# Optimization experiments

Measured on AMD Instinct MI355X. Metric: run time of the kernel, lower is better.

## Reference

```python
import jax, jax.numpy as jnp
import numpy as np

D_MODEL = 768
NUM_HEADS = 12
D_K = D_MODEL // NUM_HEADS  # 64


def setup_inputs() -> dict:
    key = jax.random.key(0)
    ks = jax.random.split(key, 7)
    B, S = 2, 4096
    Q = jax.random.normal(ks[0], (B, S, D_MODEL), dtype=jnp.float32)
    K = jax.random.normal(ks[1], (B, S, D_MODEL), dtype=jnp.float32)
    V = jax.random.normal(ks[2], (B, S, D_MODEL), dtype=jnp.float32)
    scale = 1.0 / np.sqrt(D_MODEL)
    # Per-head projection weights stacked: [H, d_model, d_k] (equivalent to
    # the torch per-head nn.Linear(d_model, d_k, bias=False) applied as x @ W)
    WQ = jax.random.normal(ks[3], (NUM_HEADS, D_MODEL, D_K), dtype=jnp.float32) * scale
    WK = jax.random.normal(ks[4], (NUM_HEADS, D_MODEL, D_K), dtype=jnp.float32) * scale
    WV = jax.random.normal(ks[5], (NUM_HEADS, D_MODEL, D_K), dtype=jnp.float32) * scale
    # Output projection: [num_head*d_v, d_model]
    WO = jax.random.normal(ks[6], (NUM_HEADS * D_K, D_MODEL), dtype=jnp.float32) * scale
    return {"Q": Q, "K": K, "V": V, "WQ": WQ, "WK": WK, "WV": WV, "WO": WO}


def reference(Q, K, V, WQ, WK, WV, WO):
    # Per-head projections (batched over heads): [B,H,S,d_k]
    q = jnp.einsum('bsd,hdk->bhsk', Q, WQ)
    k = jnp.einsum('bsd,hdk->bhsk', K, WK)
    v = jnp.einsum('bsd,hdk->bhsk', V, WV)
    # Full attention scores: [B,H,S,S]
    scores = jnp.einsum('bhqd,bhsd->bhqs', q, k) / jnp.sqrt(jnp.asarray(D_K, q.dtype))
    attn = jax.nn.softmax(scores, axis=-1)  # dropout_p=0 -> identity
    out = jnp.einsum('bhqs,bhsd->bhqd', attn, v)  # [B,H,S,d_k]
    # Concatenate heads along feature dim (head order = concat order)
    B, H, S, Dk = out.shape
    out = out.transpose(0, 2, 1, 3).reshape(B, S, H * Dk)
    return out @ WO  # [B,S,d_model]
```

## Files before the change

kernel.cpp:

```cpp
#include <hip/hip_runtime.h>
#include <hip/hip_bf16.h>
#include <stdint.h>
#include <stddef.h>

#define NH 12
#define DKH 64
#define DM 768
#define SS 4096

typedef __attribute__((ext_vector_type(8))) short bf16x8;
typedef __attribute__((ext_vector_type(4))) float f32x4;
typedef __attribute__((ext_vector_type(16))) float f32x16;

__device__ __forceinline__ unsigned short f2bf(float x) {
  union { float f; unsigned int u; } a; a.f = x;
  unsigned int r = a.u + 0x7fffu + ((a.u >> 16) & 1u);
  return (unsigned short)(r >> 16);
}

__device__ __forceinline__ unsigned pkbf2(float a, float b) {
  union { __hip_bfloat162 h; unsigned u; } x;
  x.h = __float22bfloat162_rn(float2{a, b});
  return x.u;
}

__device__ __forceinline__ unsigned cvt_pk_bf16(float lo, float hi) {
  unsigned r;
  asm("v_cvt_pk_bf16_f32 %0, %1, %2" : "=v"(r) : "v"(lo), "v"(hi));
  return r;
}

__device__ __forceinline__ void plane32_swap(unsigned& a, unsigned& b) {
  asm("v_permlane32_swap_b32 %0, %1" : "+v"(a), "+v"(b));
}

__device__ __forceinline__ float fast_exp2(float x) {
#if __has_builtin(__builtin_amdgcn_exp2f)
  return __builtin_amdgcn_exp2f(x);
#else
  return exp2f(x);
#endif
}

__device__ __forceinline__ void gload16(const void* g, void* l) {
  __builtin_amdgcn_global_load_lds(
      (const __attribute__((address_space(1))) void*)g,
      (__attribute__((address_space(3))) void*)l, 16, 0, 0);
}

__global__ __launch_bounds__(256) void conv_weights(
    const float* __restrict__ WQ, const float* __restrict__ WK,
    const float* __restrict__ WV, const float* __restrict__ WO,
    unsigned short* __restrict__ wq, unsigned short* __restrict__ wk,
    unsigned short* __restrict__ wv, unsigned short* __restrict__ wo) {
  int idx = blockIdx.x * 256 + threadIdx.x;
  if (idx >= DM * DM) return;
  int n = idx / DM, k = idx % DM;
  int src = ((n >> 6) * DM + k) * DKH + (n & 63);
  wq[idx] = f2bf(WQ[src] * 0.18033688011112042f);
  wk[idx] = f2bf(WK[src]);
  wv[idx] = f2bf(WV[src]);
  wo[idx] = f2bf(WO[k * DM + n]);
}

__global__ __launch_bounds__(256) void qkv_conv(
    const float* __restrict__ Q, const float* __restrict__ K,
    const float* __restrict__ V, unsigned short* __restrict__ out) {
  int gid = blockIdx.x * 256 + threadIdx.x;
  int t = gid / 786432, e = gid % 786432;
  const float* src = (t == 0) ? Q : (t == 1) ? K : V;
  float4 a = *(const float4*)(src + (size_t)e * 8);
  float4 c = *(const float4*)(src + (size_t)e * 8 + 4);
  union { unsigned u[4]; uint4 v; } o;
  o.u[0] = pkbf2(a.x, a.y); o.u[1] = pkbf2(a.z, a.w);
  o.u[2] = pkbf2(c.x, c.y); o.u[3] = pkbf2(c.z, c.w);
  *(uint4*)(out + (size_t)t * 6291456 + (size_t)e * 8) = o.v;
}

__global__ __launch_bounds__(256, 2) void proj_gemm3(
    const unsigned short* __restrict__ Abase,
    const unsigned short* __restrict__ Wbase,
    unsigned short* __restrict__ Obase) {
  __shared__ unsigned short As[2][128 * 64];
  __shared__ unsigned short Bs[2][96 * 64];
  const int tid = threadIdx.x;
  const int lane = tid & 63, wave = tid >> 6;
  const int wm = wave >> 1, wn = wave & 1;
  const int l15 = lane & 15, lhi = lane >> 4;
  const int lrow = lane >> 3;
  const int schunk = (lane & 7) ^ lrow;

  int fid = blockIdx.x + (blockIdx.y << 3) + (blockIdx.z << 9);
  int nid = (fid & 7) * 192 + (fid >> 3);
  const int bx = nid & 7;
  const int rem = nid >> 3;
  const int by = rem & 63, z = rem >> 6;
  const bool z2 = (z == 2);

  const unsigned short* A = Abase + (size_t)z * 6291456;
  const unsigned short* Wt = Wbase + (size_t)z * DM * DM;
  unsigned short* out = Obase + (size_t)z * 2 * NH * SS * DKH;
  const int m0 = by * 128, n0 = bx * 96;

  auto stage = [&](int k0, int buf) {
#pragma unroll
    for (int i = 0; i < 4; ++i) {
      int r = wave * 32 + i * 8;
      gload16(A + (size_t)(m0 + r + lrow) * DM + k0 + schunk * 8, &As[buf][r * 64]);
    }
#pragma unroll
    for (int i = 0; i < 3; ++i) {
      int r = wave * 24 + i * 8;
      gload16(Wt + (size_t)(n0 + r + lrow) * DM + k0 + schunk * 8, &Bs[buf][r * 64]);
    }
  };

  f32x4 acc[4][3] = {};

  stage(0, 0);
  stage(64, 1);

  for (int t = 0; t < 12; ++t) {
    if (t < 11) asm volatile("s_waitcnt vmcnt(7)" ::: "memory");
    else        asm volatile("s_waitcnt vmcnt(0)" ::: "memory");
    asm volatile("s_barrier" ::: "memory");
    const int buf = t & 1;
    bf16x8 af[4][2], bfr[3][2];
#pragma unroll
    for (int m = 0; m < 4; ++m) {
      int row = wm * 64 + m * 16 + l15;
#pragma unroll
      for (int ks = 0; ks < 2; ++ks)
        af[m][ks] = *(const bf16x8*)&As[buf][row * 64 + (((ks * 4 + lhi) ^ (row & 7)) * 8)];
    }
#pragma unroll
    for (int n = 0; n < 3; ++n) {
      int row = wn * 48 + n * 16 + l15;
#pragma unroll
      for (int ks = 0; ks < 2; ++ks)
        bfr[n][ks] = *(const bf16x8*)&Bs[buf][row * 64 + (((ks * 4 + lhi) ^ (row & 7)) * 8)];
    }
    asm volatile("s_waitcnt lgkmcnt(0)" ::: "memory");
    asm volatile("s_barrier" ::: "memory");
    if (t + 2 < 12) stage((t + 2) * 64, buf);
    __builtin_amdgcn_s_setprio(1);
#pragma unroll
    for (int ks = 0; ks < 2; ++ks)
#pragma unroll
      for (int m = 0; m < 4; ++m)
#pragma unroll
        for (int n = 0; n < 3; ++n) {
          if (z2)
            acc[m][n] = __builtin_amdgcn_mfma_f32_16x16x32_bf16(bfr[n][ks], af[m][ks], acc[m][n], 0, 0, 0);
          else
            acc[m][n] = __builtin_amdgcn_mfma_f32_16x16x32_bf16(af[m][ks], bfr[n][ks], acc[m][n], 0, 0, 0);
        }
    __builtin_amdgcn_s_setprio(0);
  }

  if (!z2) {
#pragma unroll
    for (int m = 0; m < 4; ++m) {
#pragma unroll
      for (int r = 0; r < 4; ++r) {
        int row = m0 + wm * 64 + m * 16 + lhi * 4 + r;
        int bb = row >> 12, s = row & 4095;
#pragma unroll
        for (int n = 0; n < 3; ++n) {
          int col = n0 + wn * 48 + n * 16 + l15;
          int hh = col >> 6, dk = col & 63;
          out[((size_t)(bb * NH + hh) * SS + s) * DKH + dk] = f2bf(acc[m][n][r]);
        }
      }
    }
  } else {
#pragma unroll
    for (int m = 0; m < 4; ++m) {
      int srow = m0 + wm * 64 + m * 16 + l15;
      int bb = srow >> 12, s = srow & 4095;
#pragma unroll
      for (int n = 0; n < 3; ++n) {
#pragma unroll
        for (int r = 0; r < 4; ++r) {
          int col = n0 + wn * 48 + n * 16 + lhi * 4 + r;
          int hh = col >> 6, dk = col & 63;
          out[((size_t)(bb * NH + hh) * DKH + dk) * SS + s] = f2bf(acc[m][n][r]);
        }
      }
    }
  }
}

__device__ __forceinline__ void pack_pb(const f32x16& s0, const f32x16& s1, bf16x8* pb) {
#pragma unroll
  for (int h2 = 0; h2 < 2; ++h2) {
    unsigned c0a = cvt_pk_bf16(s0[8 * h2 + 0], s0[8 * h2 + 1]);
    unsigned c1a = cvt_pk_bf16(s0[8 * h2 + 2], s0[8 * h2 + 3]);
    unsigned c0b = cvt_pk_bf16(s0[8 * h2 + 4], s0[8 * h2 + 5]);
    unsigned c1b = cvt_pk_bf16(s0[8 * h2 + 6], s0[8 * h2 + 7]);
    plane32_swap(c0a, c0b);
    plane32_swap(c1a, c1b);
    union { unsigned u[4]; bf16x8 v; } f;
    f.u[0] = c0a; f.u[1] = c1a; f.u[2] = c0b; f.u[3] = c1b;
    pb[h2] = f.v;
  }
#pragma unroll
  for (int h2 = 0; h2 < 2; ++h2) {
    unsigned c0a = cvt_pk_bf16(s1[8 * h2 + 0], s1[8 * h2 + 1]);
    unsigned c1a = cvt_pk_bf16(s1[8 * h2 + 2], s1[8 * h2 + 3]);
    unsigned c0b = cvt_pk_bf16(s1[8 * h2 + 4], s1[8 * h2 + 5]);
    unsigned c1b = cvt_pk_bf16(s1[8 * h2 + 6], s1[8 * h2 + 7]);
    plane32_swap(c0a, c0b);
    plane32_swap(c1a, c1b);
    union { unsigned u[4]; bf16x8 v; } f;
    f.u[0] = c0a; f.u[1] = c1a; f.u[2] = c0b; f.u[3] = c1b;
    pb[2 + h2] = f.v;
  }
}

__device__ __forceinline__ float tree16(const f32x16& v) {
  float a = (v[0] + v[1]) + (v[2] + v[3]);
  float b = (v[4] + v[5]) + (v[6] + v[7]);
  float c = (v[8] + v[9]) + (v[10] + v[11]);
  float d = (v[12] + v[13]) + (v[14] + v[15]);
  return (a + b) + (c + d);
}

__global__ __launch_bounds__(256, 2) void flash_attn(
    const unsigned short* __restrict__ Qp, const unsigned short* __restrict__ Kp,
    const unsigned short* __restrict__ Vt, unsigned short* __restrict__ Ao) {
  __shared__ unsigned short LDSu[2][2][8192];
  float* Ob = (float*)&LDSu[0][0][0];
  float* Lb = (float*)&LDSu[1][0][0];
  const int tid = threadIdx.x;
  const int lane = tid & 63, wave = tid >> 6;
  const int pair = wave >> 1, wp = wave & 1;
  const int ql = lane & 31, hi = lane >> 5;

  int fid = blockIdx.x + (blockIdx.y << 5);
  int nid = (fid & 7) * 96 + (fid >> 3);
  const int bx = nid & 31, bh = nid >> 5;
  const int b = bh / NH, h = bh % NH;
  const int q0 = bx * 128 + wp * 64;
  const int kvbase = pair * (SS / 2);

  bf16x8 qf0[4], qf1[4];
  {
    const unsigned short* qb = Qp + ((size_t)bh * SS + q0 + ql) * DKH;
#pragma unroll
    for (int s = 0; s < 4; ++s) {
      qf0[s] = *(const bf16x8*)(qb + s * 16 + hi * 8);
      qf1[s] = *(const bf16x8*)(qb + 32 * DKH + s * 16 + hi * 8);
    }
  }

  const unsigned short* gK = Kp + (size_t)bh * SS * DKH;
  const unsigned short* gV = Vt + (size_t)bh * DKH * SS;
  const int lrow = lane >> 3;
  const int sch = ((lane & 7) ^ lrow) * 8;
  const int xs = (ql & 7) << 3;

  unsigned short* KV0 = &LDSu[pair][0][0];
  unsigned short* KV1 = &LDSu[pair][1][0];

#pragma unroll
  for (int i = 0; i < 4; ++i) {
    int r = wp * 32 + i * 8;
    gload16(gK + (size_t)(kvbase + r + lrow) * DKH + sch, KV0 + r * 64);
    gload16(gV + (size_t)(r + lrow) * SS + kvbase + sch, KV0 + 4096 + r * 64);
  }

  f32x16 oA = {}, oB = {}, oC = {}, oD = {};
  float lp0 = 0.f, lp1 = 0.f;

  for (int it = 0; it < 32; ++it) {
    asm volatile("s_waitcnt vmcnt(0)" ::: "memory");
    __builtin_amdgcn_s_barrier();
    __builtin_amdgcn_sched_barrier(0);
    unsigned short* cur = (it & 1) ? KV1 : KV0;
    unsigned short* nxt = (it & 1) ? KV0 : KV1;
    if (it + 1 < 32) {
      int kvn = kvbase + (it + 1) * 64;
#pragma unroll
      for (int i = 0; i < 4; ++i) {
        int r = wp * 32 + i * 8;
        gload16(gK + (size_t)(kvn + r + lrow) * DKH + sch, nxt + r * 64);
        gload16(gV + (size_t)(r + lrow) * SS + kvn + sch, nxt + 4096 + r * 64);
      }
    }
    const unsigned short* Ks = cur;
    const unsigned short* Vs = cur + 4096;

    f32x16 s00 = {}, s01 = {}, s10 = {}, s11 = {};
    __builtin_amdgcn_s_setprio(1);
#pragma unroll
    for (int s = 0; s < 4; ++s) {
      bf16x8 ka0 = *(const bf16x8*)&Ks[ql * 64 + ((s * 16 + hi * 8) ^ xs)];
      bf16x8 ka1 = *(const bf16x8*)&Ks[(32 + ql) * 64 + ((s * 16 + hi * 8) ^ xs)];
      s00 = __builtin_amdgcn_mfma_f32_32x32x16_bf16(ka0, qf0[s], s00, 0, 0, 0);
      s10 = __builtin_amdgcn_mfma_f32_32x32x16_bf16(ka0, qf1[s], s10, 0, 0, 0);
      s01 = __builtin_amdgcn_mfma_f32_32x32x16_bf16(ka1, qf0[s], s01, 0, 0, 0);
      s11 = __builtin_amdgcn_mfma_f32_32x32x16_bf16(ka1, qf1[s], s11, 0, 0, 0);
    }
    __builtin_amdgcn_s_setprio(0);

#pragma unroll
    for (int r = 0; r < 16; ++r) s00[r] = fast_exp2(s00[r]);
#pragma unroll
    for (int r = 0; r < 16; ++r) s01[r] = fast_exp2(s01[r]);
#pragma unroll
    for (int r = 0; r < 16; ++r) s10[r] = fast_exp2(s10[r]);
#pragma unroll
    for (int r = 0; r < 16; ++r) s11[r] = fast_exp2(s11[r]);
    lp0 += tree16(s00) + tree16(s01);
    lp1 += tree16(s10) + tree16(s11);

    bf16x8 pb0[4], pb1[4];
    pack_pb(s00, s01, pb0);
    pack_pb(s10, s11, pb1);

    __builtin_amdgcn_s_setprio(1);
#pragma unroll
    for (int ks = 0; ks < 4; ++ks) {
      bf16x8 va0 = *(const bf16x8*)&Vs[ql * 64 + ((ks * 16 + hi * 8) ^ xs)];
      bf16x8 va1 = *(const bf16x8*)&Vs[(32 + ql) * 64 + ((ks * 16 + hi * 8) ^ xs)];
      oA = __builtin_amdgcn_mfma_f32_32x32x16_bf16(va0, pb0[ks], oA, 0, 0, 0);
      oB = __builtin_amdgcn_mfma_f32_32x32x16_bf16(va1, pb0[ks], oB, 0, 0, 0);
      oC = __builtin_amdgcn_mfma_f32_32x32x16_bf16(va0, pb1[ks], oC, 0, 0, 0);
      oD = __builtin_amdgcn_mfma_f32_32x32x16_bf16(va1, pb1[ks], oD, 0, 0, 0);
    }
    __builtin_amdgcn_s_setprio(0);
  }

  float l0 = lp0 + __shfl_xor(lp0, 32);
  float l1 = lp1 + __shfl_xor(lp1, 32);
  const int qq0 = wp * 64 + ql, qq1 = wp * 64 + 32 + ql;
  const int swz0 = (qq0 & 7) << 3, swz1 = (qq1 & 7) << 3;

  __syncthreads();
  if (pair == 0) {
#pragma unroll
    for (int g = 0; g < 4; ++g) {
      int d0 = hi * 4 + g * 8;
      *(float4*)&Ob[qq0 * 64 + (d0 ^ swz0)] = float4{oA[4 * g], oA[4 * g + 1], oA[4 * g + 2], oA[4 * g + 3]};
      *(float4*)&Ob[qq0 * 64 + ((d0 + 32) ^ swz0)] = float4{oB[4 * g], oB[4 * g + 1], oB[4 * g + 2], oB[4 * g + 3]};
      *(float4*)&Ob[qq1 * 64 + (d0 ^ swz1)] = float4{oC[4 * g], oC[4 * g + 1], oC[4 * g + 2], oC[4 * g + 3]};
      *(float4*)&Ob[qq1 * 64 + ((d0 + 32) ^ swz1)] = float4{oD[4 * g], oD[4 * g + 1], oD[4 * g + 2], oD[4 * g + 3]};
    }
    if (hi == 0) { Lb[qq0] = l0; Lb[qq1] = l1; }
  }
  __syncthreads();
  if (pair == 1) {
    float inv0 = 1.0f / (l0 + Lb[qq0]);
    float inv1 = 1.0f / (l1 + Lb[qq1]);
#pragma unroll
    for (int g = 0; g < 4; ++g) {
      int d0 = hi * 4 + g * 8;
      float4 pA = *(const float4*)&Ob[qq0 * 64 + (d0 ^ swz0)];
      float4 pB = *(const float4*)&Ob[qq0 * 64 + ((d0 + 32) ^ swz0)];
      float4 pC = *(const float4*)&Ob[qq1 * 64 + (d0 ^ swz1)];
      float4 pD = *(const float4*)&Ob[qq1 * 64 + ((d0 + 32) ^ swz1)];
      oA[4 * g] += pA.x; oA[4 * g + 1] += pA.y; oA[4 * g + 2] += pA.z; oA[4 * g + 3] += pA.w;
      oB[4 * g] += pB.x; oB[4 * g + 1] += pB.y; oB[4 * g + 2] += pB.z; oB[4 * g + 3] += pB.w;
      oC[4 * g] += pC.x; oC[4 * g + 1] += pC.y; oC[4 * g + 2] += pC.z; oC[4 * g + 3] += pC.w;
      oD[4 * g] += pD.x; oD[4 * g + 1] += pD.y; oD[4 * g + 2] += pD.z; oD[4 * g + 3] += pD.w;
    }
    unsigned short* orow0 = Ao + ((size_t)b * SS + q0 + ql) * DM + h * DKH;
    unsigned short* orow1 = Ao + ((size_t)b * SS + q0 + 32 + ql) * DM + h * DKH;
#pragma unroll
    for (int g = 0; g < 4; ++g) {
      int d0 = g * 8 + hi * 4;
      *(unsigned*)&orow0[d0]          = cvt_pk_bf16(oA[4 * g + 0] * inv0, oA[4 * g + 1] * inv0);
      *(unsigned*)&orow0[d0 + 2]      = cvt_pk_bf16(oA[4 * g + 2] * inv0, oA[4 * g + 3] * inv0);
      *(unsigned*)&orow0[32 + d0]     = cvt_pk_bf16(oB[4 * g + 0] * inv0, oB[4 * g + 1] * inv0);
      *(unsigned*)&orow0[32 + d0 + 2] = cvt_pk_bf16(oB[4 * g + 2] * inv0, oB[4 * g + 3] * inv0);
      *(unsigned*)&orow1[d0]          = cvt_pk_bf16(oC[4 * g + 0] * inv1, oC[4 * g + 1] * inv1);
      *(unsigned*)&orow1[d0 + 2]      = cvt_pk_bf16(oC[4 * g + 2] * inv1, oC[4 * g + 3] * inv1);
      *(unsigned*)&orow1[32 + d0]     = cvt_pk_bf16(oD[4 * g + 0] * inv1, oD[4 * g + 1] * inv1);
      *(unsigned*)&orow1[32 + d0 + 2] = cvt_pk_bf16(oD[4 * g + 2] * inv1, oD[4 * g + 3] * inv1);
    }
  }
}

__global__ __launch_bounds__(256, 2) void out_gemm(
    const unsigned short* __restrict__ A, const unsigned short* __restrict__ Wt,
    float* __restrict__ out) {
  __shared__ unsigned short As[2][64 * 64];
  __shared__ unsigned short Bs[2][128 * 64];
  const int tid = threadIdx.x;
  const int lane = tid & 63, wave = tid >> 6;
  const int wm = wave >> 1, wn = wave & 1;
  const int l15 = lane & 15, lhi = lane >> 4;
  const int lrow = lane >> 3;
  const int schunk = (lane & 7) ^ lrow;

  int fid = blockIdx.x + 6 * blockIdx.y;
  int nid = (fid & 7) * 96 + (fid >> 3);
  const int bx = nid % 6, by = nid / 6;
  const int m0 = by * 64, n0 = bx * 128;

  auto stage = [&](int k0, int buf) {
#pragma unroll
    for (int i = 0; i < 4; ++i) {
      int r = wave * 32 + i * 8;
      gload16(Wt + (size_t)(n0 + r + lrow) * DM + k0 + schunk * 8, &Bs[buf][r * 64]);
    }
#pragma unroll
    for (int i = 0; i < 2; ++i) {
      int r = wave * 16 + i * 8;
      gload16(A + (size_t)(m0 + r + lrow) * DM + k0 + schunk * 8, &As[buf][r * 64]);
    }
  };

  f32x4 acc[2][4] = {};
  stage(0, 0);
  stage(64, 1);

  for (int t = 0; t < 12; ++t) {
    if (t < 11) asm volatile("s_waitcnt vmcnt(6)" ::: "memory");
    else        asm volatile("s_waitcnt vmcnt(0)" ::: "memory");
    asm volatile("s_barrier" ::: "memory");
    const int buf = t & 1;
    bf16x8 af[2][2], bfr[4][2];
#pragma unroll
    for (int m = 0; m < 2; ++m) {
      int row = wm * 32 + m * 16 + l15;
#pragma unroll
      for (int ks = 0; ks < 2; ++ks)
        af[m][ks] = *(const bf16x8*)&As[buf][row * 64 + (((ks * 4 + lhi) ^ (row & 7)) * 8)];
    }
#pragma unroll
    for (int n = 0; n < 4; ++n) {
      int row = wn * 64 + n * 16 + l15;
#pragma unroll
      for (int ks = 0; ks < 2; ++ks)
        bfr[n][ks] = *(const bf16x8*)&Bs[buf][row * 64 + (((ks * 4 + lhi) ^ (row & 7)) * 8)];
    }
    asm volatile("s_waitcnt lgkmcnt(0)" ::: "memory");
    asm volatile("s_barrier" ::: "memory");
    if (t + 2 < 12) stage((t + 2) * 64, buf);
    __builtin_amdgcn_s_setprio(1);
#pragma unroll
    for (int ks = 0; ks < 2; ++ks)
#pragma unroll
      for (int m = 0; m < 2; ++m)
#pragma unroll
        for (int n = 0; n < 4; ++n)
          acc[m][n] = __builtin_amdgcn_mfma_f32_16x16x32_bf16(af[m][ks], bfr[n][ks], acc[m][n], 0, 0, 0);
    __builtin_amdgcn_s_setprio(0);
  }

#pragma unroll
  for (int m = 0; m < 2; ++m)
#pragma unroll
    for (int r = 0; r < 4; ++r) {
      int row = m0 + wm * 32 + m * 16 + lhi * 4 + r;
#pragma unroll
      for (int n = 0; n < 4; ++n) {
        int col = n0 + wn * 64 + n * 16 + l15;
        out[(size_t)row * DM + col] = acc[m][n][r];
      }
    }
}

extern "C" void kernel_launch(void* const* d_in, const int* in_sizes, int n_in,
                              void* d_out, int out_size, void* d_ws, size_t ws_size,
                              hipStream_t stream) {
  const float* Q  = (const float*)d_in[0];
  const float* K  = (const float*)d_in[1];
  const float* V  = (const float*)d_in[2];
  const float* WQ = (const float*)d_in[3];
  const float* WK = (const float*)d_in[4];
  const float* WV = (const float*)d_in[5];
  const float* WO = (const float*)d_in[6];
  char* ws = (char*)d_ws;

  const size_t WSZ = (size_t)DM * DM * 2;
  const size_t ABF = (size_t)2 * SS * DM * 2;
  unsigned short* w_base  = (unsigned short*)(ws);
  unsigned short* wo_t    = (unsigned short*)(ws + 3 * WSZ);
  unsigned short* qkv_bf  = (unsigned short*)(ws + 4 * WSZ);
  unsigned short* p_base  = (unsigned short*)(ws + 4 * WSZ + 3 * ABF);
  unsigned short* q_p  = p_base;
  unsigned short* k_p  = p_base + ABF / 2;
  unsigned short* v_t  = p_base + ABF;
  unsigned short* attn = p_base + 3 * (ABF / 2);

  conv_weights<<<(DM * DM + 255) / 256, 256, 0, stream>>>(
      WQ, WK, WV, WO, w_base, w_base + WSZ / 2, w_base + WSZ, wo_t);

  qkv_conv<<<9216, 256, 0, stream>>>(Q, K, V, qkv_bf);

  proj_gemm3<<<dim3(8, 64, 3), 256, 0, stream>>>(qkv_bf, w_base, p_base);

  flash_attn<<<dim3(SS / 128, 2 * NH), 256, 0, stream>>>(q_p, k_p, v_t, attn);

  out_gemm<<<dim3(6, 128), 256, 0, stream>>>(attn, wo_t, (float*)d_out);
}
```

Before: 206.0 us.

## Load K fragments directly into registers, stage only V through LDS

K tiles are now read from global memory straight into MFMA operand registers with a register double buffer, and only V keeps going through the LDS double buffer. The loop is unrolled by two so the K register sets alternate, and the first QK MFMA uses a zero constant accumulator. The intent is to cut LDS traffic and LDS footprint for K and drop the LDS read latency from the QK step. In exchange it adds register pressure from two K fragment sets and relies on global load latency being hidden behind the softmax and PV work.

```diff
diff --git a/kernel.cpp b/kernel.cpp
--- a/kernel.cpp
+++ b/kernel.cpp
@@ -229,9 +229,9 @@
 __global__ __launch_bounds__(256, 2) void flash_attn(
     const unsigned short* __restrict__ Qp, const unsigned short* __restrict__ Kp,
     const unsigned short* __restrict__ Vt, unsigned short* __restrict__ Ao) {
-  __shared__ unsigned short LDSu[2][2][8192];
-  float* Ob = (float*)&LDSu[0][0][0];
-  float* Lb = (float*)&LDSu[1][0][0];
+  __shared__ unsigned short Vlds[2][2][4096];
+  __shared__ float Lb[128];
+  float* Ob = (float*)&Vlds[0][0][0];
   const int tid = threadIdx.x;
   const int lane = tid & 63, wave = tid >> 6;
   const int pair = wave >> 1, wp = wave & 1;
@@ -260,47 +260,50 @@
   const int sch = ((lane & 7) ^ lrow) * 8;
   const int xs = (ql & 7) << 3;
 
-  unsigned short* KV0 = &LDSu[pair][0][0];
-  unsigned short* KV1 = &LDSu[pair][1][0];
-
-#pragma unroll
-  for (int i = 0; i < 4; ++i) {
-    int r = wp * 32 + i * 8;
-    gload16(gK + (size_t)(kvbase + r + lrow) * DKH + sch, KV0 + r * 64);
-    gload16(gV + (size_t)(r + lrow) * SS + kvbase + sch, KV0 + 4096 + r * 64);
-  }
+  unsigned short* Vb0 = &Vlds[pair][0][0];
+  unsigned short* Vb1 = &Vlds[pair][1][0];
+
+  const unsigned short* pkbase = gK + (size_t)ql * DKH + hi * 8;
+
+  auto loadK = [&](int kv0, bf16x8 (&k0)[4], bf16x8 (&k1)[4]) {
+    const unsigned short* pk = pkbase + (size_t)kv0 * DKH;
+#pragma unroll
+    for (int s = 0; s < 4; ++s) {
+      k0[s] = *(const bf16x8*)(pk + s * 16);
+      k1[s] = *(const bf16x8*)(pk + 2048 + s * 16);
+    }
+  };
+  auto stageV = [&](int kv0, unsigned short* dst) {
+#pragma unroll
+    for (int i = 0; i < 4; ++i) {
+      int r = wp * 32 + i * 8;
+      gload16(gV + (size_t)(r + lrow) * SS + kv0 + sch, dst + r * 64);
+    }
+  };
 
   f32x16 oA = {}, oB = {}, oC = {}, oD = {};
   float lp0 = 0.f, lp1 = 0.f;
-
-  for (int it = 0; it < 32; ++it) {
-    asm volatile("s_waitcnt vmcnt(0)" ::: "memory");
-    __builtin_amdgcn_s_barrier();
-    __builtin_amdgcn_sched_barrier(0);
-    unsigned short* cur = (it & 1) ? KV1 : KV0;
-    unsigned short* nxt = (it & 1) ? KV0 : KV1;
-    if (it + 1 < 32) {
-      int kvn = kvbase + (it + 1) * 64;
-#pragma unroll
-      for (int i = 0; i < 4; ++i) {
-        int r = wp * 32 + i * 8;
-        gload16(gK + (size_t)(kvn + r + lrow) * DKH + sch, nxt + r * 64);
-        gload16(gV + (size_t)(r + lrow) * SS + kvn + sch, nxt + 4096 + r * 64);
-      }
-    }
-    const unsigned short* Ks = cur;
-    const unsigned short* Vs = cur + 4096;
-
-    f32x16 s00 = {}, s01 = {}, s10 = {}, s11 = {};
+  const f32x16 zc = {};
+
+  bf16x8 kA0[4], kA1[4], kB0[4], kB1[4];
+  loadK(kvbase, kA0, kA1);
+  stageV(kvbase, Vb0);
+
+  auto body = [&](const bf16x8 (&k0)[4], const bf16x8 (&k1)[4],
+                  const unsigned short* Vs, int kvn, bool ld,
+                  bf16x8 (&n0)[4], bf16x8 (&n1)[4]) {
+    f32x16 s00, s01, s10, s11;
     __builtin_amdgcn_s_setprio(1);
-#pragma unroll
-    for (int s = 0; s < 4; ++s) {
-      bf16x8 ka0 = *(const bf16x8*)&Ks[ql * 64 + ((s * 16 + hi * 8) ^ xs)];
-      bf16x8 ka1 = *(const bf16x8*)&Ks[(32 + ql) * 64 + ((s * 16 + hi * 8) ^ xs)];
-      s00 = __builtin_amdgcn_mfma_f32_32x32x16_bf16(ka0, qf0[s], s00, 0, 0, 0);
-      s10 = __builtin_amdgcn_mfma_f32_32x32x16_bf16(ka0, qf1[s], s10, 0, 0, 0);
-      s01 = __builtin_amdgcn_mfma_f32_32x32x16_bf16(ka1, qf0[s], s01, 0, 0, 0);
-      s11 = __builtin_amdgcn_mfma_f32_32x32x16_bf16(ka1, qf1[s], s11, 0, 0, 0);
+    s00 = __builtin_amdgcn_mfma_f32_32x32x16_bf16(k0[0], qf0[0], zc, 0, 0, 0);
+    s10 = __builtin_amdgcn_mfma_f32_32x32x16_bf16(k0[0], qf1[0], zc, 0, 0, 0);
+    s01 = __builtin_amdgcn_mfma_f32_32x32x16_bf16(k1[0], qf0[0], zc, 0, 0, 0);
+    s11 = __builtin_amdgcn_mfma_f32_32x32x16_bf16(k1[0], qf1[0], zc, 0, 0, 0);
+#pragma unroll
+    for (int s = 1; s < 4; ++s) {
+      s00 = __builtin_amdgcn_mfma_f32_32x32x16_bf16(k0[s], qf0[s], s00, 0, 0, 0);
+      s10 = __builtin_amdgcn_mfma_f32_32x32x16_bf16(k0[s], qf1[s], s10, 0, 0, 0);
+      s01 = __builtin_amdgcn_mfma_f32_32x32x16_bf16(k1[s], qf0[s], s01, 0, 0, 0);
+      s11 = __builtin_amdgcn_mfma_f32_32x32x16_bf16(k1[s], qf1[s], s11, 0, 0, 0);
     }
     __builtin_amdgcn_s_setprio(0);
 
@@ -318,6 +321,8 @@
     bf16x8 pb0[4], pb1[4];
     pack_pb(s00, s01, pb0);
     pack_pb(s10, s11, pb1);
+
+    if (ld) loadK(kvn, n0, n1);
 
     __builtin_amdgcn_s_setprio(1);
 #pragma unroll
@@ -330,6 +335,20 @@
       oD = __builtin_amdgcn_mfma_f32_32x32x16_bf16(va1, pb1[ks], oD, 0, 0, 0);
     }
     __builtin_amdgcn_s_setprio(0);
+  };
+
+  for (int it = 0; it < 32; it += 2) {
+    asm volatile("s_waitcnt vmcnt(0)" ::: "memory");
+    __builtin_amdgcn_s_barrier();
+    __builtin_amdgcn_sched_barrier(0);
+    stageV(kvbase + (it + 1) * 64, Vb1);
+    body(kA0, kA1, Vb0, kvbase + (it + 1) * 64, true, kB0, kB1);
+
+    asm volatile("s_waitcnt vmcnt(0)" ::: "memory");
+    __builtin_amdgcn_s_barrier();
+    __builtin_amdgcn_sched_barrier(0);
+    if (it + 2 < 32) stageV(kvbase + (it + 2) * 64, Vb0);
+    body(kB0, kB1, Vb1, kvbase + (it + 2) * 64, it + 2 < 32, kA0, kA1);
   }
 
   float l0 = lp0 + __shfl_xor(lp0, 32);
```

Result: slower. 488.5 us (+137.1%).

## Drop split-KV wave pairs in flash attention, use 2-wave blocks over full KV

Applied to the files above, without the earlier changes.

The flash attention kernel no longer splits the KV sequence between two wave pairs that are merged through LDS at the end. Each 128-thread block of two waves now walks all 64 KV tiles itself, double-buffering through a smaller shared buffer, and normalizes its output directly. This removes the LDS partial-sum merge, the extra barriers and half the LDS footprint, at the cost of fewer waves per block and a serial KV loop twice as long per wave, which may reduce latency hiding.

```diff
diff --git a/kernel.cpp b/kernel.cpp
--- a/kernel.cpp
+++ b/kernel.cpp
@@ -226,15 +226,12 @@
   return (a + b) + (c + d);
 }
 
-__global__ __launch_bounds__(256, 2) void flash_attn(
+__global__ __launch_bounds__(128, 2) void flash_attn(
     const unsigned short* __restrict__ Qp, const unsigned short* __restrict__ Kp,
     const unsigned short* __restrict__ Vt, unsigned short* __restrict__ Ao) {
-  __shared__ unsigned short LDSu[2][2][8192];
-  float* Ob = (float*)&LDSu[0][0][0];
-  float* Lb = (float*)&LDSu[1][0][0];
+  __shared__ unsigned short KV[2][8192];
   const int tid = threadIdx.x;
-  const int lane = tid & 63, wave = tid >> 6;
-  const int pair = wave >> 1, wp = wave & 1;
+  const int lane = tid & 63, wp = tid >> 6;
   const int ql = lane & 31, hi = lane >> 5;
 
   int fid = blockIdx.x + (blockIdx.y << 5);
@@ -242,7 +239,6 @@
   const int bx = nid & 31, bh = nid >> 5;
   const int b = bh / NH, h = bh % NH;
   const int q0 = bx * 128 + wp * 64;
-  const int kvbase = pair * (SS / 2);
 
   bf16x8 qf0[4], qf1[4];
   {
@@ -260,36 +256,28 @@
   const int sch = ((lane & 7) ^ lrow) * 8;
   const int xs = (ql & 7) << 3;
 
-  unsigned short* KV0 = &LDSu[pair][0][0];
-  unsigned short* KV1 = &LDSu[pair][1][0];
-
-#pragma unroll
-  for (int i = 0; i < 4; ++i) {
-    int r = wp * 32 + i * 8;
-    gload16(gK + (size_t)(kvbase + r + lrow) * DKH + sch, KV0 + r * 64);
-    gload16(gV + (size_t)(r + lrow) * SS + kvbase + sch, KV0 + 4096 + r * 64);
-  }
+  auto stage = [&](int kv0, int buf) {
+#pragma unroll
+    for (int i = 0; i < 4; ++i) {
+      int r = wp * 32 + i * 8;
+      gload16(gK + (size_t)(kv0 + r + lrow) * DKH + sch, &KV[buf][r * 64]);
+      gload16(gV + (size_t)(r + lrow) * SS + kv0 + sch, &KV[buf][4096 + r * 64]);
+    }
+  };
+
+  stage(0, 0);
 
   f32x16 oA = {}, oB = {}, oC = {}, oD = {};
   float lp0 = 0.f, lp1 = 0.f;
 
-  for (int it = 0; it < 32; ++it) {
+  for (int it = 0; it < 64; ++it) {
     asm volatile("s_waitcnt vmcnt(0)" ::: "memory");
     __builtin_amdgcn_s_barrier();
     __builtin_amdgcn_sched_barrier(0);
-    unsigned short* cur = (it & 1) ? KV1 : KV0;
-    unsigned short* nxt = (it & 1) ? KV0 : KV1;
-    if (it + 1 < 32) {
-      int kvn = kvbase + (it + 1) * 64;
-#pragma unroll
-      for (int i = 0; i < 4; ++i) {
-        int r = wp * 32 + i * 8;
-        gload16(gK + (size_t)(kvn + r + lrow) * DKH + sch, nxt + r * 64);
-        gload16(gV + (size_t)(r + lrow) * SS + kvn + sch, nxt + 4096 + r * 64);
-      }
-    }
-    const unsigned short* Ks = cur;
-    const unsigned short* Vs = cur + 4096;
+    const int buf = it & 1;
+    if (it + 1 < 64) stage((it + 1) * 64, buf ^ 1);
+    const unsigned short* Ks = &KV[buf][0];
+    const unsigned short* Vs = &KV[buf][4096];
 
     f32x16 s00 = {}, s01 = {}, s10 = {}, s11 = {};
     __builtin_amdgcn_s_setprio(1);
@@ -332,53 +320,21 @@
     __builtin_amdgcn_s_setprio(0);
   }
 
-  float l0 = lp0 + __shfl_xor(lp0, 32);
-  float l1 = lp1 + __shfl_xor(lp1, 32);
-  const int qq0 = wp * 64 + ql, qq1 = wp * 64 + 32 + ql;
-  const int swz0 = (qq0 & 7) << 3, swz1 = (qq1 & 7) << 3;
-
-  __syncthreads();
-  if (pair == 0) {
-#pragma unroll
-    for (int g = 0; g < 4; ++g) {
-      int d0 = hi * 4 + g * 8;
-      *(float4*)&Ob[qq0 * 64 + (d0 ^ swz0)] = float4{oA[4 * g], oA[4 * g + 1], oA[4 * g + 2], oA[4 * g + 3]};
-      *(float4*)&Ob[qq0 * 64 + ((d0 + 32) ^ swz0)] = float4{oB[4 * g], oB[4 * g + 1], oB[4 * g + 2], oB[4 * g + 3]};
-      *(float4*)&Ob[qq1 * 64 + (d0 ^ swz1)] = float4{oC[4 * g], oC[4 * g + 1], oC[4 * g + 2], oC[4 * g + 3]};
-      *(float4*)&Ob[qq1 * 64 + ((d0 + 32) ^ swz1)] = float4{oD[4 * g], oD[4 * g + 1], oD[4 * g + 2], oD[4 * g + 3]};
-    }
-    if (hi == 0) { Lb[qq0] = l0; Lb[qq1] = l1; }
-  }
-  __syncthreads();
-  if (pair == 1) {
-    float inv0 = 1.0f / (l0 + Lb[qq0]);
-    float inv1 = 1.0f / (l1 + Lb[qq1]);
-#pragma unroll
-    for (int g = 0; g < 4; ++g) {
-      int d0 = hi * 4 + g * 8;
-      float4 pA = *(const float4*)&Ob[qq0 * 64 + (d0 ^ swz0)];
-      float4 pB = *(const float4*)&Ob[qq0 * 64 + ((d0 + 32) ^ swz0)];
-      float4 pC = *(const float4*)&Ob[qq1 * 64 + (d0 ^ swz1)];
-      float4 pD = *(const float4*)&Ob[qq1 * 64 + ((d0 + 32) ^ swz1)];
-      oA[4 * g] += pA.x; oA[4 * g + 1] += pA.y; oA[4 * g + 2] += pA.z; oA[4 * g + 3] += pA.w;
-      oB[4 * g] += pB.x; oB[4 * g + 1] += pB.y; oB[4 * g + 2] += pB.z; oB[4 * g + 3] += pB.w;
-      oC[4 * g] += pC.x; oC[4 * g + 1] += pC.y; oC[4 * g + 2] += pC.z; oC[4 * g + 3] += pC.w;
-      oD[4 * g] += pD.x; oD[4 * g + 1] += pD.y; oD[4 * g + 2] += pD.z; oD[4 * g + 3] += pD.w;
-    }
-    unsigned short* orow0 = Ao + ((size_t)b * SS + q0 + ql) * DM + h * DKH;
-    unsigned short* orow1 = Ao + ((size_t)b * SS + q0 + 32 + ql) * DM + h * DKH;
-#pragma unroll
-    for (int g = 0; g < 4; ++g) {
-      int d0 = g * 8 + hi * 4;
-      *(unsigned*)&orow0[d0]          = cvt_pk_bf16(oA[4 * g + 0] * inv0, oA[4 * g + 1] * inv0);
-      *(unsigned*)&orow0[d0 + 2]      = cvt_pk_bf16(oA[4 * g + 2] * inv0, oA[4 * g + 3] * inv0);
-      *(unsigned*)&orow0[32 + d0]     = cvt_pk_bf16(oB[4 * g + 0] * inv0, oB[4 * g + 1] * inv0);
-      *(unsigned*)&orow0[32 + d0 + 2] = cvt_pk_bf16(oB[4 * g + 2] * inv0, oB[4 * g + 3] * inv0);
-      *(unsigned*)&orow1[d0]          = cvt_pk_bf16(oC[4 * g + 0] * inv1, oC[4 * g + 1] * inv1);
-      *(unsigned*)&orow1[d0 + 2]      = cvt_pk_bf16(oC[4 * g + 2] * inv1, oC[4 * g + 3] * inv1);
-      *(unsigned*)&orow1[32 + d0]     = cvt_pk_bf16(oD[4 * g + 0] * inv1, oD[4 * g + 1] * inv1);
-      *(unsigned*)&orow1[32 + d0 + 2] = cvt_pk_bf16(oD[4 * g + 2] * inv1, oD[4 * g + 3] * inv1);
-    }
+  float inv0 = 1.0f / (lp0 + __shfl_xor(lp0, 32));
+  float inv1 = 1.0f / (lp1 + __shfl_xor(lp1, 32));
+  unsigned short* orow0 = Ao + ((size_t)b * SS + q0 + ql) * DM + h * DKH;
+  unsigned short* orow1 = Ao + ((size_t)b * SS + q0 + 32 + ql) * DM + h * DKH;
+#pragma unroll
+  for (int g = 0; g < 4; ++g) {
+    int d0 = g * 8 + hi * 4;
+    *(unsigned*)&orow0[d0]          = cvt_pk_bf16(oA[4 * g + 0] * inv0, oA[4 * g + 1] * inv0);
+    *(unsigned*)&orow0[d0 + 2]      = cvt_pk_bf16(oA[4 * g + 2] * inv0, oA[4 * g + 3] * inv0);
+    *(unsigned*)&orow0[32 + d0]     = cvt_pk_bf16(oB[4 * g + 0] * inv0, oB[4 * g + 1] * inv0);
+    *(unsigned*)&orow0[32 + d0 + 2] = cvt_pk_bf16(oB[4 * g + 2] * inv0, oB[4 * g + 3] * inv0);
+    *(unsigned*)&orow1[d0]          = cvt_pk_bf16(oC[4 * g + 0] * inv1, oC[4 * g + 1] * inv1);
+    *(unsigned*)&orow1[d0 + 2]      = cvt_pk_bf16(oC[4 * g + 2] * inv1, oC[4 * g + 3] * inv1);
+    *(unsigned*)&orow1[32 + d0]     = cvt_pk_bf16(oD[4 * g + 0] * inv1, oD[4 * g + 1] * inv1);
+    *(unsigned*)&orow1[32 + d0 + 2] = cvt_pk_bf16(oD[4 * g + 2] * inv1, oD[4 * g + 3] * inv1);
   }
 }
 
@@ -493,7 +449,7 @@
 
   proj_gemm3<<<dim3(8, 64, 3), 256, 0, stream>>>(qkv_bf, w_base, p_base);
 
-  flash_attn<<<dim3(SS / 128, 2 * NH), 256, 0, stream>>>(q_p, k_p, v_t, attn);
+  flash_attn<<<dim3(32, 24), 128, 0, stream>>>(q_p, k_p, v_t, attn);
 
   out_gemm<<<dim3(6, 128), 256, 0, stream>>>(attn, wo_t, (float*)d_out);
 }
```

After: 221.5 us. +7.5%, slower.
